# Performance work log

Hardware: AMD Instinct MI355X
Metric: run time of the kernel (lower is better)

## Reference

```python
import jax, jax.numpy as jnp
import numpy as np

INPUT_DIM = 1024
OUTPUT_DIM = 1024
NUM_SEGMENTS = 8
GRID_LO, GRID_HI = -1.0, 1.0


def setup_inputs() -> dict:
    key = jax.random.key(0)
    k1, k2 = jax.random.split(key)
    x = jax.random.normal(k1, (8, 2048, INPUT_DIM), dtype=jnp.float32)
    coeff = jax.random.normal(k2, (NUM_SEGMENTS + 1, OUTPUT_DIM, INPUT_DIM), dtype=jnp.float32) * 0.1
    bias = jnp.zeros((OUTPUT_DIM,), dtype=jnp.float32)
    return {"x": x, "coeff": coeff, "bias": bias}


def reference(x, coeff, bias):
    # x: (..., I); coeff: (G, O, I) with G = num_segments + 1; bias: (O,)
    batch_shape = x.shape[:-1]
    x_flat = x.reshape(-1, INPUT_DIM)                      # (B, I)
    grid = jnp.linspace(GRID_LO, GRID_HI, NUM_SEGMENTS + 1, dtype=x.dtype)  # (G,)
    h = (GRID_HI - GRID_LO) / NUM_SEGMENTS

    x_mean = jnp.mean(x_flat, axis=-1, keepdims=True)      # (B, 1)
    diff = x_mean - grid[None, :]                          # (B, G)
    w = jax.nn.relu(1.0 - jnp.abs(diff) / h)               # triangular hat weights
    w = w / (jnp.sum(w, axis=-1, keepdims=True) + 1e-8)    # (B, G)

    # Fused contraction order: avoid the (B, O, I) intermediate of the
    # original einsum chain; same math by associativity.
    t = jnp.einsum('bi,goi->bgo', x_flat, coeff)           # (B, G, O)
    out = jnp.einsum('bg,bgo->bo', w, t) + bias            # (B, O)
    return out.reshape(*batch_shape, OUTPUT_DIM)
```

## Files before the change

### kernel.cpp

```cpp
#include <hip/hip_runtime.h>
#include <math.h>

#define B_ROWS 16384
#define IDIM   1024
#define ODIM   1024
#define NGRID  9
#define MT_MAX 137
#define MPAD_MAX (MT_MAX*128)

#define RS_BLOCKS 1024
#define RS_ROWS   (B_ROWS / RS_BLOCKS)

typedef __attribute__((ext_vector_type(8))) short frag8;
typedef __attribute__((ext_vector_type(4))) float f32x4;

typedef __attribute__((address_space(1))) void gvoid;
typedef __attribute__((address_space(3))) void lvoid;

__device__ __forceinline__ void async_cp16(const void* g, void* l) {
  __builtin_amdgcn_global_load_lds((gvoid*)(void*)g, (lvoid*)l, 16, 0, 0);
}

__device__ __forceinline__ unsigned short f2bf(float f) {
  union { float f; unsigned u; } v; v.f = f;
  unsigned u = v.u;
  u += 0x7fffu + ((u >> 16) & 1u);
  return (unsigned short)(u >> 16);
}

__device__ __forceinline__ void seg_weights(float m, int& sI, float& w0, float& w1) {
  float wsum = 0.f, wg[NGRID];
#pragma unroll
  for (int g = 0; g < NGRID; g++) {
    float gv = -1.f + 0.25f * (float)g;
    float t = 1.f - fabsf(m - gv) * 4.f;
    wg[g] = t > 0.f ? t : 0.f;
    wsum += wg[g];
  }
  int s = (int)floorf((m + 1.f) * 4.f);
  s = s < 0 ? 0 : (s > 7 ? 7 : s);
  float inv = 1.f / (wsum + 1e-8f);
  sI = s;
  w0 = wg[s] * inv;
  w1 = wg[s + 1] * inv;
}

__global__ void zero_meta(int* bucket_cnt) {
  if (threadIdx.x < NGRID) bucket_cnt[threadIdx.x] = 0;
}

__global__ void row_stats(const float* __restrict__ x, float* __restrict__ w0a,
                          float* __restrict__ w1a, int* __restrict__ sidx,
                          int* __restrict__ rank, int* __restrict__ bucket_cnt) {
  __shared__ int lcnt[NGRID];
  __shared__ int base[NGRID];
  __shared__ int lrank[RS_ROWS];
  __shared__ int lseg[RS_ROWS];
  const int tid  = threadIdx.x;
  const int lane = tid & 63;
  const int wave = tid >> 6;
  if (tid < NGRID) lcnt[tid] = 0;
  __syncthreads();
  const int row0 = blockIdx.x * RS_ROWS;
#pragma unroll
  for (int it = 0; it < RS_ROWS / 4; ++it) {
    int r = it * 4 + wave;
    int b = row0 + r;
    const float4* xr = (const float4*)(x + (size_t)b * IDIM);
    float s = 0.f;
#pragma unroll
    for (int j = 0; j < 4; j++) {
      float4 v = xr[lane + j * 64];
      s += v.x + v.y + v.z + v.w;
    }
#pragma unroll
    for (int off = 32; off; off >>= 1) s += __shfl_down(s, off, 64);
    if (lane == 0) {
      float m = s * (1.0f / (float)IDIM);
      int sI; float w0, w1;
      seg_weights(m, sI, w0, w1);
      w0a[b] = w0; w1a[b] = w1; sidx[b] = sI;
      lseg[r] = sI;
      lrank[r] = atomicAdd(&lcnt[sI], 1);
    }
  }
  __syncthreads();
  if (tid < NGRID) base[tid] = lcnt[tid] ? atomicAdd(&bucket_cnt[tid], lcnt[tid]) : 0;
  __syncthreads();
  if (tid < RS_ROWS) rank[row0 + tid] = base[lseg[tid]] + lrank[tid];
}

#define BA_ROWS   8
#define BA_BLOCKS (B_ROWS / BA_ROWS)
#define CV_BLOCKS (NGRID * ODIM * IDIM / 4 / 256)
__global__ void build_and_cvt(const float* __restrict__ x, const float* __restrict__ coeff,
                              const float* __restrict__ w0a, const float* __restrict__ w1a,
                              const int* __restrict__ sidx, const int* __restrict__ rank,
                              const int* __restrict__ bucket_cnt,
                              unsigned short* __restrict__ Xs, float2* __restrict__ ws,
                              int* __restrict__ row_idx, unsigned short* __restrict__ Cb) {
  const int tid = threadIdx.x;
  if (blockIdx.x >= BA_BLOCKS) {
    int i = (blockIdx.x - BA_BLOCKS) * 256 + tid;
    float4 v = ((const float4*)coeff)[i];
    ushort4 o;
    o.x = f2bf(v.x); o.y = f2bf(v.y); o.z = f2bf(v.z); o.w = f2bf(v.w);
    ((ushort4*)Cb)[i] = o;
    return;
  }
  __shared__ int soffs[NGRID];
  if (tid == 0) {
    int off = 0;
#pragma unroll
    for (int g = 0; g < NGRID; g++) { soffs[g] = off; off += ((bucket_cnt[g] + 127) >> 7) << 7; }
  }
  __syncthreads();
  const int b0 = blockIdx.x * BA_ROWS;
#pragma unroll
  for (int r = 0; r < BA_ROWS; r++) {
    int b = b0 + r;
    int s = sidx[b];
    int p = soffs[s] + rank[b];
    if (tid == 0) { row_idx[p] = b; ws[p] = make_float2(w0a[b], w1a[b]); }
    float4 v = ((const float4*)(x + (size_t)b * IDIM))[tid];
    ushort4 u;
    u.x = f2bf(v.x); u.y = f2bf(v.y); u.z = f2bf(v.z); u.w = f2bf(v.w);
    *(ushort4*)(Xs + (size_t)p * IDIM + tid * 4) = u;
  }
}

__global__ void __launch_bounds__(256, 2)
kan_gemm(const unsigned short* __restrict__ Xs,
         const unsigned short* __restrict__ Cb,
         const int* __restrict__ row_idx,
         const int* __restrict__ bucket_cnt,
         const float2* __restrict__ ws,
         const float* __restrict__ bias,
         float* __restrict__ out) {
  const int mt = blockIdx.y;
  int seg = -1, pend = 0;
  {
    int off = 0;
#pragma unroll
    for (int g = 0; g < NGRID; g++) {
      int c  = bucket_cnt[g];
      int nt = (c + 127) >> 7;
      int t0 = off >> 7;
      if (mt >= t0 && mt < t0 + nt) { seg = g; pend = off + c; }
      off += nt << 7;
    }
  }
  if (seg < 0) return;

  __shared__ unsigned short As[2][128 * 32];
  __shared__ unsigned short Bs0[2][128 * 32];
  __shared__ unsigned short Bs1[2][128 * 32];

  const int tid  = threadIdx.x;
  const int lane = tid & 63;
  const int wave = tid >> 6;
  const int wm   = wave >> 1;
  const int wn   = wave & 1;
  const size_t rowA0 = (size_t)mt * 128;
  const int    colB0 = blockIdx.x * 128;

  const int lrow = lane >> 2;
  const int lk8  = (lane & 3) * 8;

  const unsigned short* gA  = Xs + (rowA0 + lrow) * IDIM + lk8;
  const unsigned short* gB0 = Cb + ((size_t)(seg * ODIM + colB0 + lrow)) * IDIM + lk8;
  const unsigned short* gB1 = gB0 + (size_t)ODIM * IDIM;

  f32x4 acc0[4][4] = {};
  f32x4 acc1[4][4] = {};

  for (int kk = 0; kk < IDIM; kk += 64) {
    __syncthreads();
#pragma unroll
    for (int h = 0; h < 2; h++) {
#pragma unroll
      for (int t = 0; t < 2; t++) {
        int r0 = (wave * 2 + t) * 16;
        int ko = kk + h * 32;
        async_cp16(gA  + (size_t)r0 * IDIM + ko, &As[h][r0 * 32]);
        async_cp16(gB0 + (size_t)r0 * IDIM + ko, &Bs0[h][r0 * 32]);
        async_cp16(gB1 + (size_t)r0 * IDIM + ko, &Bs1[h][r0 * 32]);
      }
    }
    __syncthreads();

#pragma unroll
    for (int h = 0; h < 2; h++) {
      frag8 af[4], bfr[4];
#pragma unroll
      for (int mi = 0; mi < 4; mi++)
        af[mi] = *(const frag8*)&As[h][(wm * 64 + mi * 16 + (lane & 15)) * 32 + (lane >> 4) * 8];
#pragma unroll
      for (int ni = 0; ni < 4; ni++)
        bfr[ni] = *(const frag8*)&Bs0[h][(wn * 64 + ni * 16 + (lane & 15)) * 32 + (lane >> 4) * 8];
#pragma unroll
      for (int mi = 0; mi < 4; mi++)
#pragma unroll
        for (int ni = 0; ni < 4; ni++)
          acc0[mi][ni] = __builtin_amdgcn_mfma_f32_16x16x32_bf16(af[mi], bfr[ni], acc0[mi][ni], 0, 0, 0);
#pragma unroll
      for (int ni = 0; ni < 4; ni++)
        bfr[ni] = *(const frag8*)&Bs1[h][(wn * 64 + ni * 16 + (lane & 15)) * 32 + (lane >> 4) * 8];
#pragma unroll
      for (int mi = 0; mi < 4; mi++)
#pragma unroll
        for (int ni = 0; ni < 4; ni++)
          acc1[mi][ni] = __builtin_amdgcn_mfma_f32_16x16x32_bf16(af[mi], bfr[ni], acc1[mi][ni], 0, 0, 0);
    }
  }

  int   col[4]; float bv[4];
#pragma unroll
  for (int ni = 0; ni < 4; ni++) {
    col[ni] = colB0 + wn * 64 + ni * 16 + (lane & 15);
    bv[ni]  = bias[col[ni]];
  }
#pragma unroll
  for (int mi = 0; mi < 4; mi++) {
    int prow = (int)rowA0 + wm * 64 + mi * 16 + (lane >> 4) * 4;
#pragma unroll
    for (int r = 0; r < 4; r++) {
      int p = prow + r;
      if (p < pend) {
        int orow = row_idx[p];
        float2 w = ws[p];
        float* o = out + (size_t)orow * ODIM;
#pragma unroll
        for (int ni = 0; ni < 4; ni++)
          o[col[ni]] = w.x * acc0[mi][ni][r] + w.y * acc1[mi][ni][r] + bv[ni];
      }
    }
  }
}

__global__ void fallback_kernel(const float* __restrict__ x, const float* __restrict__ coeff,
                                const float* __restrict__ bias, float* __restrict__ out) {
  int b = blockIdx.x;
  int tid = threadIdx.x;
  __shared__ float xs[IDIM];
  __shared__ float ps[4];
  __shared__ float mw[2];
  __shared__ int   ms;
  float4 v = ((const float4*)(x + (size_t)b * IDIM))[tid];
  ((float4*)xs)[tid] = v;
  float s = v.x + v.y + v.z + v.w;
#pragma unroll
  for (int off = 32; off; off >>= 1) s += __shfl_down(s, off, 64);
  if ((tid & 63) == 0) ps[tid >> 6] = s;
  __syncthreads();
  if (tid == 0) {
    float m = (ps[0] + ps[1] + ps[2] + ps[3]) * (1.0f / (float)IDIM);
    int sI; float w0, w1;
    seg_weights(m, sI, w0, w1);
    mw[0] = w0; mw[1] = w1; ms = sI;
  }
  __syncthreads();
  float w0 = mw[0], w1 = mw[1]; int sI = ms;
  for (int o = tid; o < ODIM; o += 256) {
    const float* c0 = coeff + ((size_t)sI * ODIM + o) * IDIM;
    const float* c1 = c0 + (size_t)ODIM * IDIM;
    float a0 = 0.f, a1 = 0.f;
    for (int i = 0; i < IDIM; i++) { a0 += xs[i] * c0[i]; a1 += xs[i] * c1[i]; }
    out[(size_t)b * ODIM + o] = w0 * a0 + w1 * a1 + bias[o];
  }
}

extern "C" void kernel_launch(void* const* d_in, const int* in_sizes, int n_in,
                              void* d_out, int out_size, void* d_ws, size_t ws_size,
                              hipStream_t stream) {
  const float* x     = (const float*)d_in[0];
  const float* coeff = (const float*)d_in[1];
  const float* bias  = (const float*)d_in[2];
  float* out = (float*)d_out;

  size_t szXs = (size_t)MPAD_MAX * IDIM * sizeof(unsigned short);
  size_t szCb = (size_t)NGRID * ODIM * IDIM * sizeof(unsigned short);
  size_t o0 = 0;
  unsigned short* Xs = (unsigned short*)((char*)d_ws + o0); o0 += szXs;
  unsigned short* Cb = (unsigned short*)((char*)d_ws + o0); o0 += szCb;
  float2* ws = (float2*)((char*)d_ws + o0); o0 += (size_t)MPAD_MAX * 8;
  float* w0a = (float*)((char*)d_ws + o0); o0 += (size_t)B_ROWS * 4;
  float* w1a = (float*)((char*)d_ws + o0); o0 += (size_t)B_ROWS * 4;
  int* sidx  = (int*)((char*)d_ws + o0);   o0 += (size_t)B_ROWS * 4;
  int* rank  = (int*)((char*)d_ws + o0);   o0 += (size_t)B_ROWS * 4;
  int* row_idx = (int*)((char*)d_ws + o0); o0 += (size_t)MPAD_MAX * 4;
  int* bucket_cnt = (int*)((char*)d_ws + o0); o0 += 256;

  if (ws_size < o0) {
    fallback_kernel<<<B_ROWS, 256, 0, stream>>>(x, coeff, bias, out);
    return;
  }

  zero_meta<<<1, 64, 0, stream>>>(bucket_cnt);
  row_stats<<<RS_BLOCKS, 256, 0, stream>>>(x, w0a, w1a, sidx, rank, bucket_cnt);
  build_and_cvt<<<BA_BLOCKS + CV_BLOCKS, 256, 0, stream>>>(x, coeff, w0a, w1a, sidx, rank,
                                                           bucket_cnt, Xs, ws, row_idx, Cb);
  kan_gemm<<<dim3(ODIM / 128, MT_MAX), 256, 0, stream>>>(Xs, Cb, row_idx, bucket_cnt, ws, bias, out);
}
```

Before: 271.5 us.

## Fuse x bf16 conversion into row stats, gather rows in GEMM, skip unused coeff planes

```diff
diff --git a/kernel.cpp b/kernel.cpp
--- a/kernel.cpp
+++ b/kernel.cpp
@@ -5,11 +5,12 @@
 #define IDIM   1024
 #define ODIM   1024
 #define NGRID  9
-#define MT_MAX 137
-#define MPAD_MAX (MT_MAX*128)
 
 #define RS_BLOCKS 1024
 #define RS_ROWS   (B_ROWS / RS_BLOCKS)
+
+#define GEMM_GROUPS 18
+#define GEMM_BLOCKS (GEMM_GROUPS * 64)
 
 typedef __attribute__((ext_vector_type(8))) short frag8;
 typedef __attribute__((ext_vector_type(4))) float f32x4;
@@ -49,9 +50,11 @@
   if (threadIdx.x < NGRID) bucket_cnt[threadIdx.x] = 0;
 }
 
-__global__ void row_stats(const float* __restrict__ x, float* __restrict__ w0a,
-                          float* __restrict__ w1a, int* __restrict__ sidx,
-                          int* __restrict__ rank, int* __restrict__ bucket_cnt) {
+__global__ void row_stats_fused(const float* __restrict__ x,
+                                unsigned short* __restrict__ Xb,
+                                float2* __restrict__ ws2,
+                                int* __restrict__ seg_rows,
+                                int* __restrict__ bucket_cnt) {
   __shared__ int lcnt[NGRID];
   __shared__ int base[NGRID];
   __shared__ int lrank[RS_ROWS];
@@ -67,11 +70,19 @@
     int r = it * 4 + wave;
     int b = row0 + r;
     const float4* xr = (const float4*)(x + (size_t)b * IDIM);
+    ushort4* xw = (ushort4*)(Xb + (size_t)b * IDIM);
+    float4 v[4];
     float s = 0.f;
 #pragma unroll
     for (int j = 0; j < 4; j++) {
-      float4 v = xr[lane + j * 64];
-      s += v.x + v.y + v.z + v.w;
+      v[j] = xr[lane + j * 64];
+      s += v[j].x + v[j].y + v[j].z + v[j].w;
+    }
+#pragma unroll
+    for (int j = 0; j < 4; j++) {
+      ushort4 u;
+      u.x = f2bf(v[j].x); u.y = f2bf(v[j].y); u.z = f2bf(v[j].z); u.w = f2bf(v[j].w);
+      xw[lane + j * 64] = u;
     }
 #pragma unroll
     for (int off = 32; off; off >>= 1) s += __shfl_down(s, off, 64);
@@ -79,7 +90,7 @@
       float m = s * (1.0f / (float)IDIM);
       int sI; float w0, w1;
       seg_weights(m, sI, w0, w1);
-      w0a[b] = w0; w1a[b] = w1; sidx[b] = sI;
+      ws2[b] = make_float2(w0, w1);
       lseg[r] = sI;
       lrank[r] = atomicAdd(&lcnt[sI], 1);
     }
@@ -87,70 +98,51 @@
   __syncthreads();
   if (tid < NGRID) base[tid] = lcnt[tid] ? atomicAdd(&bucket_cnt[tid], lcnt[tid]) : 0;
   __syncthreads();
-  if (tid < RS_ROWS) rank[row0 + tid] = base[lseg[tid]] + lrank[tid];
-}
-
-#define BA_ROWS   8
-#define BA_BLOCKS (B_ROWS / BA_ROWS)
-#define CV_BLOCKS (NGRID * ODIM * IDIM / 4 / 256)
-__global__ void build_and_cvt(const float* __restrict__ x, const float* __restrict__ coeff,
-                              const float* __restrict__ w0a, const float* __restrict__ w1a,
-                              const int* __restrict__ sidx, const int* __restrict__ rank,
-                              const int* __restrict__ bucket_cnt,
-                              unsigned short* __restrict__ Xs, float2* __restrict__ ws,
-                              int* __restrict__ row_idx, unsigned short* __restrict__ Cb) {
-  const int tid = threadIdx.x;
-  if (blockIdx.x >= BA_BLOCKS) {
-    int i = (blockIdx.x - BA_BLOCKS) * 256 + tid;
-    float4 v = ((const float4*)coeff)[i];
-    ushort4 o;
-    o.x = f2bf(v.x); o.y = f2bf(v.y); o.z = f2bf(v.z); o.w = f2bf(v.w);
-    ((ushort4*)Cb)[i] = o;
-    return;
-  }
-  __shared__ int soffs[NGRID];
-  if (tid == 0) {
-    int off = 0;
-#pragma unroll
-    for (int g = 0; g < NGRID; g++) { soffs[g] = off; off += ((bucket_cnt[g] + 127) >> 7) << 7; }
-  }
-  __syncthreads();
-  const int b0 = blockIdx.x * BA_ROWS;
-#pragma unroll
-  for (int r = 0; r < BA_ROWS; r++) {
-    int b = b0 + r;
-    int s = sidx[b];
-    int p = soffs[s] + rank[b];
-    if (tid == 0) { row_idx[p] = b; ws[p] = make_float2(w0a[b], w1a[b]); }
-    float4 v = ((const float4*)(x + (size_t)b * IDIM))[tid];
-    ushort4 u;
-    u.x = f2bf(v.x); u.y = f2bf(v.y); u.z = f2bf(v.z); u.w = f2bf(v.w);
-    *(ushort4*)(Xs + (size_t)p * IDIM + tid * 4) = u;
-  }
+  if (tid < RS_ROWS)
+    seg_rows[lseg[tid] * B_ROWS + base[lseg[tid]] + lrank[tid]] = row0 + tid;
+}
+
+#define CV_BLKS_PER_PLANE (ODIM * IDIM / 4 / 256)
+__global__ void cvt_coeff(const float* __restrict__ c, unsigned short* __restrict__ cb,
+                          const int* __restrict__ bucket_cnt) {
+  const int g  = blockIdx.x >> 10;
+  const int cI = blockIdx.x & 1023;
+  bool need = bucket_cnt[g] > 0;
+  if (!need && g > 0) need = bucket_cnt[g - 1] > 0;
+  if (!need) return;
+  int i = (g * CV_BLKS_PER_PLANE + cI) * 256 + threadIdx.x;
+  float4 v = ((const float4*)c)[i];
+  ushort4 o;
+  o.x = f2bf(v.x); o.y = f2bf(v.y); o.z = f2bf(v.z); o.w = f2bf(v.w);
+  ((ushort4*)cb)[i] = o;
 }
 
 __global__ void __launch_bounds__(256, 2)
-kan_gemm(const unsigned short* __restrict__ Xs,
+kan_gemm(const unsigned short* __restrict__ Xb,
          const unsigned short* __restrict__ Cb,
-         const int* __restrict__ row_idx,
+         const int* __restrict__ seg_rows,
          const int* __restrict__ bucket_cnt,
-         const float2* __restrict__ ws,
+         const float2* __restrict__ ws2,
          const float* __restrict__ bias,
          float* __restrict__ out) {
-  const int mt = blockIdx.y;
-  int seg = -1, pend = 0;
+  const int sub = blockIdx.x & 63;
+  const int mt  = (blockIdx.x >> 6) * 8 + (sub & 7);
+  const int nt  = sub >> 3;
+
+  int seg = -1, lt = 0, cnt = 0;
   {
-    int off = 0;
+    int t0 = 0;
 #pragma unroll
     for (int g = 0; g < NGRID; g++) {
-      int c  = bucket_cnt[g];
-      int nt = (c + 127) >> 7;
-      int t0 = off >> 7;
-      if (mt >= t0 && mt < t0 + nt) { seg = g; pend = off + c; }
-      off += nt << 7;
+      int c   = bucket_cnt[g];
+      int ntg = (c + 127) >> 7;
+      if (mt >= t0 && mt < t0 + ntg) { seg = g; lt = mt - t0; cnt = c; }
+      t0 += ntg;
     }
   }
   if (seg < 0) return;
+  const int rlim = cnt - lt * 128;
+  const int* rows = seg_rows + seg * B_ROWS + lt * 128;
 
   __shared__ unsigned short As[2][128 * 32];
   __shared__ unsigned short Bs0[2][128 * 32];
@@ -161,13 +153,18 @@
   const int wave = tid >> 6;
   const int wm   = wave >> 1;
   const int wn   = wave & 1;
-  const size_t rowA0 = (size_t)mt * 128;
-  const int    colB0 = blockIdx.x * 128;
+  const int colB0 = nt * 128;
 
   const int lrow = lane >> 2;
   const int lk8  = (lane & 3) * 8;
 
-  const unsigned short* gA  = Xs + (rowA0 + lrow) * IDIM + lk8;
+  int rid[2];
+#pragma unroll
+  for (int t = 0; t < 2; t++) {
+    int idx = (wave * 2 + t) * 16 + lrow;
+    rid[t] = rows[idx < rlim ? idx : rlim - 1];
+  }
+
   const unsigned short* gB0 = Cb + ((size_t)(seg * ODIM + colB0 + lrow)) * IDIM + lk8;
   const unsigned short* gB1 = gB0 + (size_t)ODIM * IDIM;
 
@@ -178,11 +175,11 @@
     __syncthreads();
 #pragma unroll
     for (int h = 0; h < 2; h++) {
+      int ko = kk + h * 32;
 #pragma unroll
       for (int t = 0; t < 2; t++) {
         int r0 = (wave * 2 + t) * 16;
-        int ko = kk + h * 32;
-        async_cp16(gA  + (size_t)r0 * IDIM + ko, &As[h][r0 * 32]);
+        async_cp16(Xb + (size_t)rid[t] * IDIM + ko + lk8, &As[h][r0 * 32]);
         async_cp16(gB0 + (size_t)r0 * IDIM + ko, &Bs0[h][r0 * 32]);
         async_cp16(gB1 + (size_t)r0 * IDIM + ko, &Bs1[h][r0 * 32]);
       }
@@ -222,13 +219,13 @@
   }
 #pragma unroll
   for (int mi = 0; mi < 4; mi++) {
-    int prow = (int)rowA0 + wm * 64 + mi * 16 + (lane >> 4) * 4;
+    int irow = wm * 64 + mi * 16 + (lane >> 4) * 4;
 #pragma unroll
     for (int r = 0; r < 4; r++) {
-      int p = prow + r;
-      if (p < pend) {
-        int orow = row_idx[p];
-        float2 w = ws[p];
+      int idx = irow + r;
+      if (idx < rlim) {
+        int orow = rows[idx];
+        float2 w = ws2[orow];
         float* o = out + (size_t)orow * ODIM;
 #pragma unroll
         for (int ni = 0; ni < 4; ni++)
@@ -278,17 +275,13 @@
   const float* bias  = (const float*)d_in[2];
   float* out = (float*)d_out;
 
-  size_t szXs = (size_t)MPAD_MAX * IDIM * sizeof(unsigned short);
+  size_t szXb = (size_t)B_ROWS * IDIM * sizeof(unsigned short);
   size_t szCb = (size_t)NGRID * ODIM * IDIM * sizeof(unsigned short);
   size_t o0 = 0;
-  unsigned short* Xs = (unsigned short*)((char*)d_ws + o0); o0 += szXs;
+  unsigned short* Xb = (unsigned short*)((char*)d_ws + o0); o0 += szXb;
   unsigned short* Cb = (unsigned short*)((char*)d_ws + o0); o0 += szCb;
-  float2* ws = (float2*)((char*)d_ws + o0); o0 += (size_t)MPAD_MAX * 8;
-  float* w0a = (float*)((char*)d_ws + o0); o0 += (size_t)B_ROWS * 4;
-  float* w1a = (float*)((char*)d_ws + o0); o0 += (size_t)B_ROWS * 4;
-  int* sidx  = (int*)((char*)d_ws + o0);   o0 += (size_t)B_ROWS * 4;
-  int* rank  = (int*)((char*)d_ws + o0);   o0 += (size_t)B_ROWS * 4;
-  int* row_idx = (int*)((char*)d_ws + o0); o0 += (size_t)MPAD_MAX * 4;
+  float2* ws2 = (float2*)((char*)d_ws + o0); o0 += (size_t)B_ROWS * 8;
+  int* seg_rows = (int*)((char*)d_ws + o0); o0 += (size_t)NGRID * B_ROWS * 4;
   int* bucket_cnt = (int*)((char*)d_ws + o0); o0 += 256;
 
   if (ws_size < o0) {
@@ -297,8 +290,7 @@
   }
 
   zero_meta<<<1, 64, 0, stream>>>(bucket_cnt);
-  row_stats<<<RS_BLOCKS, 256, 0, stream>>>(x, w0a, w1a, sidx, rank, bucket_cnt);
-  build_and_cvt<<<BA_BLOCKS + CV_BLOCKS, 256, 0, stream>>>(x, coeff, w0a, w1a, sidx, rank,
-                                                           bucket_cnt, Xs, ws, row_idx, Cb);
-  kan_gemm<<<dim3(ODIM / 128, MT_MAX), 256, 0, stream>>>(Xs, Cb, row_idx, bucket_cnt, ws, bias, out);
-}
+  row_stats_fused<<<RS_BLOCKS, 256, 0, stream>>>(x, Xb, ws2, seg_rows, bucket_cnt);
+  cvt_coeff<<<NGRID * CV_BLKS_PER_PLANE, 256, 0, stream>>>(coeff, Cb, bucket_cnt);
+  kan_gemm<<<GEMM_BLOCKS, 256, 0, stream>>>(Xb, Cb, seg_rows, bucket_cnt, ws2, bias, out);
+}
```

After: 247.1 us. 9.0% less time.
